# Optimization experiments

Measured on AMD Instinct MI355X. Metric: run time of the kernel, lower is better.

## Reference

```python
import jax, jax.numpy as jnp
import numpy as np

E = 8           # num experts
TOPK = 2
NUM_TOKENS = 4096
K = 2048        # hidden dim
N = 2816        # intermediate dim
P = NUM_TOKENS * TOPK   # num_valid_tokens (token, expert-slot) pairs
PE = P // E             # pairs per expert (token-sorted, equal load)


def setup_inputs() -> dict:
    key = jax.random.key(0)
    ks = jax.random.split(key, 6)
    x = jax.random.normal(ks[0], (NUM_TOKENS, K), dtype=jnp.float32)
    W1 = jax.random.normal(ks[1], (E, N, K), dtype=jnp.float32) * (K ** -0.5)  # gate proj
    W3 = jax.random.normal(ks[2], (E, N, K), dtype=jnp.float32) * (K ** -0.5)  # up proj
    W2 = jax.random.normal(ks[3], (E, K, N), dtype=jnp.float32) * (N ** -0.5)  # down proj
    topk_weights = jax.random.uniform(ks[4], (P,), dtype=jnp.float32)          # router weights per pair
    sorted_token_ids = jax.random.randint(ks[5], (P,), 0, NUM_TOKENS, dtype=jnp.int32)
    # token-sorted dispatch: pairs grouped by expert, equal count per expert
    expert_ids = jnp.repeat(jnp.arange(E, dtype=jnp.int32), PE)
    return {"x": x, "W1": W1, "W3": W3, "W2": W2,
            "topk_weights": topk_weights,
            "sorted_token_ids": sorted_token_ids,
            "expert_ids": expert_ids}


def reference(x, W1, W3, W2, topk_weights, sorted_token_ids, expert_ids):
    # Pairs are grouped by expert (token-sorted dispatch), PE pairs per expert.
    eids = expert_ids.reshape(E, PE)[:, 0]            # expert id per group
    xg = x[sorted_token_ids].reshape(E, PE, K)        # gather token activations per pair
    gate = jnp.einsum('epk,enk->epn', xg, W1[eids])   # [E, PE, N]
    up = jnp.einsum('epk,enk->epn', xg, W3[eids])     # [E, PE, N]
    # kernel computes sigmoid(gate) * up (as written in the triton body)
    h = jax.nn.sigmoid(gate) * up
    out_p = jnp.einsum('epn,ekn->epk', h, W2[eids])   # down proj, [E, PE, K]
    out_p = out_p * topk_weights.reshape(E, PE, 1)
    # scatter-add per-pair results into per-token output (atomic_add in kernel)
    out = jnp.zeros((x.shape[0], K), dtype=x.dtype)
    out = out.at[sorted_token_ids].add(out_p.reshape(P, K))
    return out
```

## Files before the change

### kernel.cpp

```cpp
#include <hip/hip_runtime.h>
#include <hip/hip_bf16.h>
#include <cstdint>

typedef __bf16 bf16_t;
typedef __attribute__((ext_vector_type(8))) __bf16 bf16x8;
typedef __attribute__((ext_vector_type(4))) __bf16 bf16x4;
typedef __attribute__((ext_vector_type(4))) float f32x4;

#define NEXP 8
#define DK   2048
#define DN   2816
#define DN2  5632
#define NP   8192
#define PPE  1024

__global__ void k_cvt_w13(const float* __restrict__ W1, const float* __restrict__ W3,
                          bf16_t* __restrict__ dst) {
    const int total4 = NEXP * DN * (DK / 4);
    int stride = gridDim.x * blockDim.x;
    for (int i = blockIdx.x * blockDim.x + threadIdx.x; i < 2 * total4; i += stride) {
        int sel = i >= total4;
        int j   = sel ? i - total4 : i;
        int g   = j >> 9;
        int c4  = j & 511;
        int e   = g / DN;
        int n   = g - e * DN;
        long drow = (long)e * DN2 + ((n >> 4) << 5) + (n & 15) + (sel ? 16 : 0);
        float4 v = reinterpret_cast<const float4*>(sel ? W3 : W1)[j];
        bf16x4 o = { (bf16_t)v.x, (bf16_t)v.y, (bf16_t)v.z, (bf16_t)v.w };
        *reinterpret_cast<bf16x4*>(dst + drow * DK + c4 * 4) = o;
    }
}

__global__ void k_cvt(const float* __restrict__ src, bf16_t* __restrict__ dst, int total4) {
    int stride = gridDim.x * blockDim.x;
    for (int i = blockIdx.x * blockDim.x + threadIdx.x; i < total4; i += stride) {
        float4 v = reinterpret_cast<const float4*>(src)[i];
        bf16x4 o = { (bf16_t)v.x, (bf16_t)v.y, (bf16_t)v.z, (bf16_t)v.w };
        reinterpret_cast<bf16x4*>(dst)[i] = o;
    }
}

__global__ void k_gather(const float* __restrict__ x, const int* __restrict__ ids,
                         bf16_t* __restrict__ xg) {
    int i = blockIdx.x * blockDim.x + threadIdx.x;
    if (i >= NP * (DK / 4)) return;
    int p  = i >> 9;
    int c4 = i & 511;
    int tok = ids[p];
    float4 v = reinterpret_cast<const float4*>(x + (size_t)tok * DK)[c4];
    bf16x4 o = { (bf16_t)v.x, (bf16_t)v.y, (bf16_t)v.z, (bf16_t)v.w };
    *reinterpret_cast<bf16x4*>(xg + (size_t)p * DK + c4 * 4) = o;
}

__device__ __forceinline__ void gl2lds16(const bf16_t* g, bf16_t* l) {
    __builtin_amdgcn_global_load_lds(
        (__attribute__((address_space(1))) void*)(const_cast<bf16_t*>(g)),
        (__attribute__((address_space(3))) void*)(l), 16, 0, 0);
}

#define BARX() __builtin_amdgcn_s_barrier()
#define LGKM0() asm volatile("s_waitcnt lgkmcnt(0)" ::: "memory")
#define VMW4() asm volatile("s_waitcnt vmcnt(4)" ::: "memory")
#define VMW0() asm volatile("s_waitcnt vmcnt(0)" ::: "memory")

#define STG(ARR, SRC, LD, BUF, HALF, KT) do {                                   \
    gl2lds16((SRC) + (long)((HALF) * 128) * (LD) + (long)(KT) * 64,             \
             &ARR[BUF][(HALF) * 128 + w8][0]);                                  \
    gl2lds16((SRC) + (long)((HALF) * 128 + 64) * (LD) + (long)(KT) * 64,        \
             &ARR[BUF][(HALF) * 128 + 64 + w8][0]);                             \
} while (0)

#define LOADA(DST, BASE) do { _Pragma("unroll")                                 \
    for (int mi_ = 0; mi_ < 4; ++mi_) {                                         \
        DST[mi_][0] = *reinterpret_cast<const bf16x8*>((BASE) + aoff0 + mi_ * 1024); \
        DST[mi_][1] = *reinterpret_cast<const bf16x8*>((BASE) + aoff1 + mi_ * 1024); \
    } } while (0)

#define LOADB(DST, BASE) do { _Pragma("unroll")                                 \
    for (int ni_ = 0; ni_ < 2; ++ni_) {                                         \
        DST[ni_][0] = *reinterpret_cast<const bf16x8*>((BASE) + boff0 + ni_ * 1024); \
        DST[ni_][1] = *reinterpret_cast<const bf16x8*>((BASE) + boff1 + ni_ * 1024); \
    } } while (0)

#define MFMAQ(AF, BF, MIB, NIB) do {                                            \
    __builtin_amdgcn_s_setprio(1);                                              \
    _Pragma("unroll") for (int kk_ = 0; kk_ < 2; ++kk_)                         \
    _Pragma("unroll") for (int mi_ = 0; mi_ < 4; ++mi_)                         \
    _Pragma("unroll") for (int ni_ = 0; ni_ < 2; ++ni_)                         \
        acc[(MIB) + mi_][(NIB) + ni_] = __builtin_amdgcn_mfma_f32_16x16x32_bf16( \
            AF[mi_][kk_], BF[ni_][kk_], acc[(MIB) + mi_][(NIB) + ni_], 0, 0, 0); \
    __builtin_amdgcn_s_setprio(0);                                              \
} while (0)

template <int EPI>
__launch_bounds__(512, 2)
__global__ void k_gemm(const bf16_t* __restrict__ A, const bf16_t* __restrict__ B,
                       bf16_t* __restrict__ Hout, float* __restrict__ Fout,
                       const float* __restrict__ tw, const int* __restrict__ ids,
                       int Mtiles, int Ntiles, int nkt, int lda, int ldb,
                       long aStride, long bStride) {
    __shared__ bf16_t As[2][256][64];
    __shared__ bf16_t Bs[2][256][64];

    const int nwg = gridDim.x;
    const int logical = (blockIdx.x & 7) * (nwg >> 3) + (blockIdx.x >> 3);
    const int tpe = Mtiles * Ntiles;
    const int e  = logical / tpe;
    const int r  = logical - e * tpe;
    const int nt = r / Mtiles;
    const int mt = r - nt * Mtiles;

    const int tid  = threadIdx.x;
    const int w    = tid >> 6;
    const int w8   = w * 8;
    const int lane = tid & 63;
    const int wr = w >> 2, wc = w & 3;
    const int fr = lane & 15;
    const int fc = lane >> 4;

    const int srow = tid >> 3;
    const int schk = (tid & 7) ^ (srow & 7);
    const bf16_t* aSrc = A + (long)e * aStride + ((long)mt * 256 + srow) * lda + schk * 8;
    const bf16_t* bSrc = B + (long)e * bStride + ((long)nt * 256 + srow) * ldb + schk * 8;

    const int sx = lane & 7;
    const int aoff0 = (wr * 128 + fr) * 64 + ((0 + fc) ^ sx) * 8;
    const int aoff1 = (wr * 128 + fr) * 64 + ((4 + fc) ^ sx) * 8;
    const int boff0 = (wc * 64 + fr) * 64 + ((0 + fc) ^ sx) * 8;
    const int boff1 = (wc * 64 + fr) * 64 + ((4 + fc) ^ sx) * 8;

    const bf16_t* As0 = &As[0][0][0];
    const bf16_t* As1 = &As[1][0][0];
    const bf16_t* Bs0 = &Bs[0][0][0];
    const bf16_t* Bs1 = &Bs[1][0][0];

    f32x4 acc[8][4];
#pragma unroll
    for (int a = 0; a < 8; ++a)
#pragma unroll
        for (int b = 0; b < 4; ++b) acc[a][b] = (f32x4){0.f, 0.f, 0.f, 0.f};

    bf16x8 af[4][2], ah[4][2], bl[2][2], bh[2][2];

    STG(As, aSrc, lda, 0, 0, 0); STG(As, aSrc, lda, 0, 1, 0);
    STG(Bs, bSrc, ldb, 0, 0, 0); STG(Bs, bSrc, ldb, 0, 1, 0);
    STG(Bs, bSrc, ldb, 1, 0, 1); STG(Bs, bSrc, ldb, 1, 1, 1);
    VMW4();
    BARX();

    const int nIter = nkt >> 1;
    for (int it = 0; it < nIter; ++it) {
        const int t = it * 2;
        const bool last = (it == nIter - 1);
        LOADA(af, As0); LOADB(bl, Bs0);
        STG(As, aSrc, lda, 1, 0, t + 1);
        BARX(); LGKM0();
        MFMAQ(af, bl, 0, 0);
        BARX();
        LOADB(bh, Bs0 + 2048);
        STG(As, aSrc, lda, 1, 1, t + 1);
        BARX(); LGKM0();
        MFMAQ(af, bh, 0, 2);
        BARX();
        LOADA(ah, As0 + 4096);
        if (!last) STG(Bs, bSrc, ldb, 0, 0, t + 2);
        BARX(); LGKM0();
        MFMAQ(ah, bh, 4, 2);
        BARX();
        if (!last) { STG(Bs, bSrc, ldb, 0, 1, t + 2); VMW4(); } else { VMW0(); }
        BARX();
        MFMAQ(ah, bl, 4, 0);
        BARX();
        LOADA(af, As1); LOADB(bl, Bs1);
        if (!last) STG(As, aSrc, lda, 0, 0, t + 2);
        BARX(); LGKM0();
        MFMAQ(af, bl, 0, 0);
        BARX();
        LOADB(bh, Bs1 + 2048);
        if (!last) STG(As, aSrc, lda, 0, 1, t + 2);
        BARX(); LGKM0();
        MFMAQ(af, bh, 0, 2);
        BARX();
        LOADA(ah, As1 + 4096);
        if (!last) STG(Bs, bSrc, ldb, 1, 0, t + 3);
        BARX(); LGKM0();
        MFMAQ(ah, bh, 4, 2);
        BARX();
        if (!last) { STG(Bs, bSrc, ldb, 1, 1, t + 3); VMW4(); } else { VMW0(); }
        BARX();
        MFMAQ(ah, bl, 4, 0);
        BARX();
    }

    if constexpr (EPI == 0) {
        const long prow0 = (long)e * PPE + (long)mt * 256 + wr * 128 + fc * 4;
        const int col0 = nt * 128 + wc * 32 + fr;
#pragma unroll
        for (int mi = 0; mi < 8; ++mi)
#pragma unroll
            for (int i = 0; i < 4; ++i) {
                long row = prow0 + mi * 16 + i;
#pragma unroll
                for (int p = 0; p < 2; ++p) {
                    float g = acc[mi][2 * p][i];
                    float u = acc[mi][2 * p + 1][i];
                    float s = 1.f / (1.f + __expf(-g));
                    Hout[row * DN + col0 + p * 16] = (bf16_t)(s * u);
                }
            }
    } else {
        const int p0 = e * PPE + mt * 256 + wr * 128 + fc * 4;
        const int col0 = nt * 256 + wc * 64 + fr;
#pragma unroll
        for (int mi = 0; mi < 8; ++mi)
#pragma unroll
            for (int i = 0; i < 4; ++i) {
                int gp = p0 + mi * 16 + i;
                float wgt = tw[gp];
                float* ob = Fout + (long)ids[gp] * DK + col0;
#pragma unroll
                for (int ni = 0; ni < 4; ++ni)
                    atomicAdd(ob + ni * 16, acc[mi][ni][i] * wgt);
            }
    }
}

extern "C" void kernel_launch(void* const* d_in, const int* in_sizes, int n_in,
                              void* d_out, int out_size, void* d_ws, size_t ws_size,
                              hipStream_t stream) {
    const float* x   = (const float*)d_in[0];
    const float* W1  = (const float*)d_in[1];
    const float* W3  = (const float*)d_in[2];
    const float* W2  = (const float*)d_in[3];
    const float* tw  = (const float*)d_in[4];
    const int*   sid = (const int*)d_in[5];
    float* out = (float*)d_out;

    char* ws = (char*)d_ws;
    bf16_t* w13i = (bf16_t*)ws;
    bf16_t* w2b  = (bf16_t*)(ws + 184549376L);
    bf16_t* xg   = (bf16_t*)(ws + 276824064L);
    bf16_t* h    = (bf16_t*)(ws + 310378496L);

    hipMemsetAsync(d_out, 0, (size_t)out_size * sizeof(float), stream);

    k_cvt_w13<<<2048, 256, 0, stream>>>(W1, W3, w13i);
    k_cvt<<<2048, 256, 0, stream>>>(W2, w2b, NEXP * DK * (DN / 4));
    k_gather<<<NP * (DK / 4) / 256, 256, 0, stream>>>(x, sid, xg);

    k_gemm<0><<<NEXP * 4 * 22, 512, 0, stream>>>(
        xg, w13i, h, nullptr, nullptr, nullptr,
        4, 22, 32, DK, DK, (long)PPE * DK, (long)DN2 * DK);

    k_gemm<1><<<NEXP * 4 * 8, 512, 0, stream>>>(
        h, w2b, nullptr, out, tw, sid,
        4, 8, 44, DN, DN, (long)PPE * DN, (long)DK * DN);
}
```

Baseline: 519.0 us.

## Restructure GEMM main loop to prefetch full tiles and overlap LDS reads with MFMA

Rewrites the double-buffered GEMM main loop so that the next LDS fragment loads are issued right before the MFMA groups that consume earlier fragments, and whole A/B tiles for step t+2 are staged into the freed buffer in one burst. Explicit lgkmcnt waits before each MFMA group are dropped, and the last-iteration branches are removed by clamping the prefetch index (redundant reloads at the tail). The tile-index mapping also changes to iterate N-tiles fastest within an M-tile, which alters L2 reuse of the A/B operands. Risks include correctness if the compiler does not insert the needed LDS waits, plus extra wasted loads at the end.

```diff
diff --git a/kernel.cpp b/kernel.cpp
--- a/kernel.cpp
+++ b/kernel.cpp
@@ -61,7 +61,6 @@
 
 #define BARX() __builtin_amdgcn_s_barrier()
 #define LGKM0() asm volatile("s_waitcnt lgkmcnt(0)" ::: "memory")
-#define VMW4() asm volatile("s_waitcnt vmcnt(4)" ::: "memory")
 #define VMW0() asm volatile("s_waitcnt vmcnt(0)" ::: "memory")
 
 #define STG(ARR, SRC, LD, BUF, HALF, KT) do {                                   \
@@ -69,6 +68,9 @@
              &ARR[BUF][(HALF) * 128 + w8][0]);                                  \
     gl2lds16((SRC) + (long)((HALF) * 128 + 64) * (LD) + (long)(KT) * 64,        \
              &ARR[BUF][(HALF) * 128 + 64 + w8][0]);                             \
+} while (0)
+#define STGF(ARR, SRC, LD, BUF, KT) do {                                        \
+    STG(ARR, SRC, LD, BUF, 0, KT); STG(ARR, SRC, LD, BUF, 1, KT);               \
 } while (0)
 
 #define LOADA(DST, BASE) do { _Pragma("unroll")                                 \
@@ -108,8 +110,8 @@
     const int tpe = Mtiles * Ntiles;
     const int e  = logical / tpe;
     const int r  = logical - e * tpe;
-    const int nt = r / Mtiles;
-    const int mt = r - nt * Mtiles;
+    const int mt = r / Ntiles;
+    const int nt = r - mt * Ntiles;
 
     const int tid  = threadIdx.x;
     const int w    = tid >> 6;
@@ -143,55 +145,49 @@
 
     bf16x8 af[4][2], ah[4][2], bl[2][2], bh[2][2];
 
-    STG(As, aSrc, lda, 0, 0, 0); STG(As, aSrc, lda, 0, 1, 0);
-    STG(Bs, bSrc, ldb, 0, 0, 0); STG(Bs, bSrc, ldb, 0, 1, 0);
-    STG(Bs, bSrc, ldb, 1, 0, 1); STG(Bs, bSrc, ldb, 1, 1, 1);
-    VMW4();
+    const int last = nkt - 1;
+
+    STGF(As, aSrc, lda, 0, 0); STGF(Bs, bSrc, ldb, 0, 0);
+    STGF(As, aSrc, lda, 1, 1); STGF(Bs, bSrc, ldb, 1, 1);
+    VMW0();
     BARX();
+    LOADA(af, As0); LOADB(bl, Bs0);
 
     const int nIter = nkt >> 1;
     for (int it = 0; it < nIter; ++it) {
         const int t = it * 2;
-        const bool last = (it == nIter - 1);
+        const int tc2 = t + 2 < last ? t + 2 : last;
+        const int tc3 = t + 3 < last ? t + 3 : last;
+        LOADB(bh, Bs0 + 2048);
+        BARX();
+        MFMAQ(af, bl, 0, 0);
+        LOADA(ah, As0 + 4096);
+        BARX();
+        MFMAQ(af, bh, 0, 2);
+        BARX();
+        MFMAQ(ah, bl, 4, 0);
+        VMW0();
+        BARX();
+        LOADA(af, As1); LOADB(bl, Bs1);
+        STGF(Bs, bSrc, ldb, 0, tc2); STGF(As, aSrc, lda, 0, tc2);
+        BARX();
+        MFMAQ(ah, bh, 4, 2);
+        LOADB(bh, Bs1 + 2048);
+        BARX();
+        MFMAQ(af, bl, 0, 0);
+        LOADA(ah, As1 + 4096);
+        BARX();
+        MFMAQ(af, bh, 0, 2);
+        BARX();
+        MFMAQ(ah, bl, 4, 0);
+        VMW0();
+        BARX();
         LOADA(af, As0); LOADB(bl, Bs0);
-        STG(As, aSrc, lda, 1, 0, t + 1);
-        BARX(); LGKM0();
-        MFMAQ(af, bl, 0, 0);
-        BARX();
-        LOADB(bh, Bs0 + 2048);
-        STG(As, aSrc, lda, 1, 1, t + 1);
-        BARX(); LGKM0();
-        MFMAQ(af, bh, 0, 2);
-        BARX();
-        LOADA(ah, As0 + 4096);
-        if (!last) STG(Bs, bSrc, ldb, 0, 0, t + 2);
-        BARX(); LGKM0();
+        STGF(Bs, bSrc, ldb, 1, tc3); STGF(As, aSrc, lda, 1, tc3);
+        BARX();
         MFMAQ(ah, bh, 4, 2);
-        BARX();
-        if (!last) { STG(Bs, bSrc, ldb, 0, 1, t + 2); VMW4(); } else { VMW0(); }
-        BARX();
-        MFMAQ(ah, bl, 4, 0);
-        BARX();
-        LOADA(af, As1); LOADB(bl, Bs1);
-        if (!last) STG(As, aSrc, lda, 0, 0, t + 2);
-        BARX(); LGKM0();
-        MFMAQ(af, bl, 0, 0);
-        BARX();
-        LOADB(bh, Bs1 + 2048);
-        if (!last) STG(As, aSrc, lda, 0, 1, t + 2);
-        BARX(); LGKM0();
-        MFMAQ(af, bh, 0, 2);
-        BARX();
-        LOADA(ah, As1 + 4096);
-        if (!last) STG(Bs, bSrc, ldb, 1, 0, t + 3);
-        BARX(); LGKM0();
-        MFMAQ(ah, bh, 4, 2);
-        BARX();
-        if (!last) { STG(Bs, bSrc, ldb, 1, 1, t + 3); VMW4(); } else { VMW0(); }
-        BARX();
-        MFMAQ(ah, bl, 4, 0);
-        BARX();
-    }
+    }
+    VMW0(); LGKM0();
 
     if constexpr (EPI == 0) {
         const long prow0 = (long)e * PPE + (long)mt * 256 + wr * 128 + fc * 4;
```

Measured after the change: 549.2 us. +5.8%, slower.
